# Performance work log

Measured on AMD Instinct MI355X. Metric: run time of the kernel, lower is better.

The kernel has to match this reference:

```python
import jax, jax.numpy as jnp
import numpy as np

EMBED_DIM = 128
NUM_HEADS = 4
WH, WW = 7, 7
N = WH * WW
HEAD_DIM = EMBED_DIM // NUM_HEADS
SCALE = HEAD_DIM ** -0.5


def _rel_position_index():
    # double_step_seq(2*Ww-1, Wh, 1, Ww), then idx = coords + coords.T, flip cols
    seq1 = np.arange(0, (2 * WW - 1) * WH, 2 * WW - 1)
    seq2 = np.arange(0, WW)
    coords = (seq1[:, None] + seq2[None, :]).reshape(1, -1)  # (1, N)
    idx = coords + coords.T                                   # (N, N)
    idx = idx[:, ::-1].copy()                                 # flip(1)
    return jnp.asarray(idx, dtype=jnp.int32)

REL_IDX = _rel_position_index()


def setup_inputs() -> dict:
    key = jax.random.key(0)
    ks = jax.random.split(key, 8)
    B = 4096
    nW = 64
    C = EMBED_DIM
    x = jax.random.normal(ks[0], (B, N, C), dtype=jnp.float32)
    # shift mask: values in (-inf, 0]; emulate with -100 on ~half the entries
    mask = jnp.where(jax.random.uniform(ks[1], (nW, N, N)) > 0.5, -100.0, 0.0).astype(jnp.float32)
    lim = 1.0 / np.sqrt(C)
    qkv_w = jax.random.uniform(ks[2], (3 * C, C), minval=-lim, maxval=lim, dtype=jnp.float32)
    qkv_b = jax.random.uniform(ks[3], (3 * C,), minval=-lim, maxval=lim, dtype=jnp.float32)
    proj_w = jax.random.uniform(ks[4], (C, C), minval=-lim, maxval=lim, dtype=jnp.float32)
    proj_b = jax.random.uniform(ks[5], (C,), minval=-lim, maxval=lim, dtype=jnp.float32)
    n_rel = (2 * WH - 1) * (2 * WW - 1)
    bias_table = 0.02 * jax.random.normal(ks[6], (n_rel, NUM_HEADS), dtype=jnp.float32)
    return {"x": x, "mask": mask, "qkv_w": qkv_w, "qkv_b": qkv_b,
            "proj_w": proj_w, "proj_b": proj_b, "bias_table": bias_table}


def reference(x, mask, qkv_w, qkv_b, proj_w, proj_b, bias_table):
    B, n, C = x.shape
    H, D = NUM_HEADS, HEAD_DIM
    qkv = x @ qkv_w.T + qkv_b                       # (B, N, 3C)
    qkv = qkv.reshape(B, n, 3, H, D).transpose(2, 0, 3, 1, 4)
    q, k, v = qkv[0], qkv[1], qkv[2]                # each (B, H, N, D)
    attn = jnp.einsum('bhnd,bhmd->bhnm', q * SCALE, k)
    # relative position bias gather: (N, N, H) -> (H, N, N)
    rel_bias = bias_table[REL_IDX.reshape(-1)].reshape(n, n, H).transpose(2, 0, 1)
    attn = attn + rel_bias[None]
    nW = mask.shape[0]
    attn = attn.reshape(B // nW, nW, H, n, n) + mask[None, :, None]
    attn = attn.reshape(B, H, n, n)
    attn = jax.nn.softmax(attn, axis=-1)
    out = jnp.einsum('bhnm,bhmd->bhnd', attn, v)    # (B, H, N, D)
    out = out.transpose(0, 2, 1, 3).reshape(B, n, C)
    return out @ proj_w.T + proj_b
```

## Files before the change

### kernel.cpp

```cpp
#include <hip/hip_runtime.h>


typedef __bf16 bf16_t;
typedef __bf16 bf8v  __attribute__((ext_vector_type(8)));
typedef __bf16 bf4v  __attribute__((ext_vector_type(4)));
typedef float  f4v   __attribute__((ext_vector_type(4)));

#define QK_SCALE 0.17677669529663687f

__device__ __forceinline__ f4v mfma16(bf8v a, bf8v b, f4v c) {
  return __builtin_amdgcn_mfma_f32_16x16x32_bf16(a, b, c, 0, 0, 0);
}

__device__ __forceinline__ bf8v join8(bf4v lo, bf4v hi) {
  return __builtin_shufflevector(lo, hi, 0, 1, 2, 3, 4, 5, 6, 7);
}

__global__ void prep_kernel(const float* __restrict__ mask,
                            const float* __restrict__ qkv_w,
                            const float* __restrict__ proj_w,
                            const float* __restrict__ bias_table,
                            bf16_t* __restrict__ wq,
                            bf16_t* __restrict__ wp,
                            float* __restrict__ cbs) {
  const int stride = gridDim.x * blockDim.x;
  const int tid0 = blockIdx.x * blockDim.x + threadIdx.x;
  for (int i = tid0; i < 24 * 4 * 64 * 8; i += stride) {
    int j = i & 7, l = (i >> 3) & 63, kt = (i >> 9) & 3, t = i >> 11;
    int n = t * 16 + (l & 15), k = kt * 32 + (l >> 4) * 8 + j;
    wq[i] = (bf16_t)qkv_w[n * 128 + k];
  }
  for (int i = tid0; i < 8 * 4 * 64 * 8; i += stride) {
    int j = i & 7, l = (i >> 3) & 63, kt = (i >> 9) & 3, t = i >> 11;
    int n = t * 16 + (l & 15), k = kt * 32 + (l >> 4) * 8 + j;
    wp[i] = (bf16_t)proj_w[n * 128 + k];
  }
  for (int i = tid0; i < 64 * 4 * 64 * 64; i += stride) {
    int j = i & 63;
    int l16 = j >> 2, nt = j & 3;
    int m = nt * 16 + l16;
    int n = (i >> 6) & 63, h = (i >> 12) & 3, w = i >> 14;
    float v;
    if (m >= 49) {
      v = -1e30f;
    } else if (n >= 49) {
      v = 0.0f;
    } else {
      int cn = 13 * (n / 7) + n % 7;
      int mm = 48 - m;
      int cm = 13 * (mm / 7) + mm % 7;
      v = bias_table[(cn + cm) * 4 + h] + mask[(w * 49 + n) * 49 + m];
    }
    cbs[i] = v;
  }
}

__global__ __launch_bounds__(256, 3) void msa_kernel(
    const float* __restrict__ x,
    const float* __restrict__ qkv_b,
    const float* __restrict__ proj_b,
    const bf16_t* __restrict__ wq,
    const bf16_t* __restrict__ wp,
    const float* __restrict__ cbs,
    float* __restrict__ out) {
  __shared__ __align__(16) bf16_t gA[8704];
  __shared__ __align__(16) bf16_t gB[4][4608];

#define AS(r, c)   gA[(r) * 136 + (c)]
#define VT(h, d, t) gA[((h) * 32 + (d)) * 68 + (t)]
#define QQ(h, r, d) gB[h][(r) * 36 + (d)]
#define KK(h, r, d) gB[h][2304 + (r) * 36 + (d)]
#define PP(h, n, m) gB[h][(n) * 72 + (m)]
#define OV(h, t, d) gB[h][(t) * 36 + (d)]

  const int tid = threadIdx.x;
  const int wv  = tid >> 6;
  const int ln  = tid & 63;
  const int l16 = ln & 15;
  const int l4  = ln >> 4;
  const int b   = blockIdx.x;
  const int w   = b & 63;

  {
    const float4* xb = (const float4*)(x + (size_t)b * (49 * 128));
    for (int i = tid; i < 64 * 32; i += 256) {
      int r = i >> 5, c4 = (i & 31) << 2;
      float4 v;
      if (r < 49) v = xb[(r * 128 + c4) >> 2];
      else        v = make_float4(0.f, 0.f, 0.f, 0.f);
      bf4v o = { (bf16_t)v.x, (bf16_t)v.y, (bf16_t)v.z, (bf16_t)v.w };
      *(bf4v*)&AS(r, c4) = o;
    }
  }
  __syncthreads();

  {
    f4v acc[4][6];
    for (int mt = 0; mt < 4; ++mt)
      for (int nj = 0; nj < 6; ++nj) acc[mt][nj] = (f4v){0.f, 0.f, 0.f, 0.f};
    for (int kt = 0; kt < 4; ++kt) {
      bf8v a[4];
      for (int mt = 0; mt < 4; ++mt)
        a[mt] = *(const bf8v*)&AS(mt * 16 + l16, kt * 32 + l4 * 8);
      bf8v bwv[6];
      for (int nj = 0; nj < 6; ++nj) {
        int t = wv * 6 + nj;
        bwv[nj] = *(const bf8v*)(wq + (((t * 4 + kt) * 64 + ln) << 3));
      }
      for (int mt = 0; mt < 4; ++mt)
        for (int nj = 0; nj < 6; ++nj)
          acc[mt][nj] = mfma16(a[mt], bwv[nj], acc[mt][nj]);
    }
    __syncthreads();
    for (int nj = 0; nj < 6; ++nj) {
      int t = wv * 6 + nj;
      int n0 = t * 16 + l16;
      float bias = qkv_b[n0];
      int sect = n0 >> 7;
      int h = (n0 & 127) >> 5;
      int d = n0 & 31;
      for (int mt = 0; mt < 4; ++mt) {
        int row0 = mt * 16 + l4 * 4;
        if (sect == 0) {
          for (int r = 0; r < 4; ++r)
            QQ(h, row0 + r, d) = (bf16_t)((acc[mt][nj][r] + bias) * QK_SCALE);
        } else if (sect == 1) {
          for (int r = 0; r < 4; ++r)
            KK(h, row0 + r, d) = (bf16_t)(acc[mt][nj][r] + bias);
        } else {
          bf4v o = { (bf16_t)(acc[mt][nj][0] + bias), (bf16_t)(acc[mt][nj][1] + bias),
                     (bf16_t)(acc[mt][nj][2] + bias), (bf16_t)(acc[mt][nj][3] + bias) };
          *(bf4v*)&VT(h, d, row0) = o;
        }
      }
    }
  }
  __syncthreads();

  {
    const int h = wv;
    f4v lg[4][4];
    bf8v qf[4], kf[4];
    for (int mt = 0; mt < 4; ++mt) {
      bf4v lo = *(const bf4v*)&QQ(h, mt * 16 + l16, l4 * 8);
      bf4v hi = *(const bf4v*)&QQ(h, mt * 16 + l16, l4 * 8 + 4);
      qf[mt] = join8(lo, hi);
    }
    for (int nt = 0; nt < 4; ++nt) {
      bf4v lo = *(const bf4v*)&KK(h, nt * 16 + l16, l4 * 8);
      bf4v hi = *(const bf4v*)&KK(h, nt * 16 + l16, l4 * 8 + 4);
      kf[nt] = join8(lo, hi);
    }
    for (int mt = 0; mt < 4; ++mt)
      for (int nt = 0; nt < 4; ++nt)
        lg[mt][nt] = mfma16(qf[mt], kf[nt], (f4v){0.f, 0.f, 0.f, 0.f});

    const float* cbp = cbs + ((size_t)(w * 4 + h) << 12);
    for (int mt = 0; mt < 4; ++mt) {
      for (int r = 0; r < 4; ++r) {
        int row = mt * 16 + l4 * 4 + r;
        float4 cbv = *(const float4*)(cbp + (row << 6) + l16 * 4);
        float vals[4];
        vals[0] = __expf(fmaxf(lg[mt][0][r] + cbv.x, -80.f));
        vals[1] = __expf(fmaxf(lg[mt][1][r] + cbv.y, -80.f));
        vals[2] = __expf(fmaxf(lg[mt][2][r] + cbv.z, -80.f));
        vals[3] = __expf(fmaxf(lg[mt][3][r] + cbv.w, -80.f));
        float s = (vals[0] + vals[1]) + (vals[2] + vals[3]);
        for (int off = 1; off < 16; off <<= 1) s += __shfl_xor(s, off);
        float inv = 1.0f / s;
        for (int nt = 0; nt < 4; ++nt)
          PP(h, row, nt * 16 + l16) = (bf16_t)(vals[nt] * inv);
      }
    }

    f4v oc[2][4];
    for (int mt = 0; mt < 2; ++mt)
      for (int nt = 0; nt < 4; ++nt) oc[mt][nt] = (f4v){0.f, 0.f, 0.f, 0.f};
    for (int ks = 0; ks < 2; ++ks) {
      bf8v vf[2], pf[4];
      for (int mt = 0; mt < 2; ++mt) {
        bf4v lo = *(const bf4v*)&VT(h, mt * 16 + l16, ks * 32 + l4 * 8);
        bf4v hi = *(const bf4v*)&VT(h, mt * 16 + l16, ks * 32 + l4 * 8 + 4);
        vf[mt] = join8(lo, hi);
      }
      for (int nt = 0; nt < 4; ++nt)
        pf[nt] = *(const bf8v*)&PP(h, nt * 16 + l16, ks * 32 + l4 * 8);
      for (int mt = 0; mt < 2; ++mt)
        for (int nt = 0; nt < 4; ++nt)
          oc[mt][nt] = mfma16(vf[mt], pf[nt], oc[mt][nt]);
    }
    for (int mt = 0; mt < 2; ++mt)
      for (int nt = 0; nt < 4; ++nt) {
        bf4v o = { (bf16_t)oc[mt][nt][0], (bf16_t)oc[mt][nt][1],
                   (bf16_t)oc[mt][nt][2], (bf16_t)oc[mt][nt][3] };
        *(bf4v*)&OV(h, nt * 16 + l16, mt * 16 + l4 * 4) = o;
      }
  }
  __syncthreads();

  {
    f4v acc[4][2];
    for (int mt = 0; mt < 4; ++mt)
      for (int nj = 0; nj < 2; ++nj) acc[mt][nj] = (f4v){0.f, 0.f, 0.f, 0.f};
    for (int kt = 0; kt < 4; ++kt) {
      bf8v a[4];
      for (int mt = 0; mt < 4; ++mt) {
        bf4v lo = *(const bf4v*)&OV(kt, mt * 16 + l16, l4 * 8);
        bf4v hi = *(const bf4v*)&OV(kt, mt * 16 + l16, l4 * 8 + 4);
        a[mt] = join8(lo, hi);
      }
      bf8v bwv[2];
      for (int nj = 0; nj < 2; ++nj) {
        int t = wv * 2 + nj;
        bwv[nj] = *(const bf8v*)(wp + (((t * 4 + kt) * 64 + ln) << 3));
      }
      for (int mt = 0; mt < 4; ++mt)
        for (int nj = 0; nj < 2; ++nj)
          acc[mt][nj] = mfma16(a[mt], bwv[nj], acc[mt][nj]);
    }
    float* ob = out + (size_t)b * (49 * 128);
    for (int nj = 0; nj < 2; ++nj) {
      int c = (wv * 2 + nj) * 16 + l16;
      float pb = proj_b[c];
      for (int mt = 0; mt < 4; ++mt) {
        for (int r = 0; r < 4; ++r) {
          int row = mt * 16 + l4 * 4 + r;
          if (row < 49) ob[row * 128 + c] = acc[mt][nj][r] + pb;
        }
      }
    }
  }
}

extern "C" void kernel_launch(void* const* d_in, const int* in_sizes, int n_in,
                              void* d_out, int out_size, void* d_ws, size_t ws_size,
                              hipStream_t stream) {
  const float* x          = (const float*)d_in[0];
  const float* mask       = (const float*)d_in[1];
  const float* qkv_w      = (const float*)d_in[2];
  const float* qkv_b      = (const float*)d_in[3];
  const float* proj_w     = (const float*)d_in[4];
  const float* proj_b     = (const float*)d_in[5];
  const float* bias_table = (const float*)d_in[6];

  char* ws = (char*)d_ws;
  bf16_t* wq = (bf16_t*)ws;
  bf16_t* wp = (bf16_t*)(ws + 98304);
  float*  cbs = (float*)(ws + 131072);

  prep_kernel<<<1024, 256, 0, stream>>>(mask, qkv_w, proj_w, bias_table, wq, wp, cbs);
  msa_kernel<<<4096, 256, 0, stream>>>(x, qkv_b, proj_b, wq, wp, cbs, (float*)d_out);
}
```

Before: 293.6 us.

## Assign QKV columns per head to each wave and swizzle shared-memory layouts

Each wave now computes the Q, K and V columns for its own head directly from x loaded from global memory into registers, instead of staging x in LDS and spreading QKV columns across waves. This removes the x staging buffer and two block-wide barriers, since each wave only reads its own head's LDS region until the projection stage. Padded LDS layouts are replaced with XOR-swizzled layouts so 16-byte fragment loads replace split 8-byte loads. Every wave now reads x from global or cache separately, and the qkv_b loads and LDS footprint change.

```diff
diff --git a/kernel.cpp b/kernel.cpp
--- a/kernel.cpp
+++ b/kernel.cpp
@@ -12,9 +12,9 @@
   return __builtin_amdgcn_mfma_f32_16x16x32_bf16(a, b, c, 0, 0, 0);
 }
 
-__device__ __forceinline__ bf8v join8(bf4v lo, bf4v hi) {
-  return __builtin_shufflevector(lo, hi, 0, 1, 2, 3, 4, 5, 6, 7);
-}
+#define QIX(row, d) ((row) * 32 + ((((((d) >> 3) ^ (((row) >> 1) & 3)) & 3)) << 3) + ((d) & 7))
+#define VIX(dd, t)  (4096 + (dd) * 64 + ((((((t) >> 3) ^ ((dd) & 7)) & 7)) << 3) + ((t) & 7))
+#define PIX(n, m)   ((n) * 64 + ((((((m) >> 3) ^ ((n) & 7)) & 7)) << 3) + ((m) & 7))
 
 __global__ void prep_kernel(const float* __restrict__ mask,
                             const float* __restrict__ qkv_w,
@@ -63,15 +63,7 @@
     const bf16_t* __restrict__ wp,
     const float* __restrict__ cbs,
     float* __restrict__ out) {
-  __shared__ __align__(16) bf16_t gA[8704];
-  __shared__ __align__(16) bf16_t gB[4][4608];
-
-#define AS(r, c)   gA[(r) * 136 + (c)]
-#define VT(h, d, t) gA[((h) * 32 + (d)) * 68 + (t)]
-#define QQ(h, r, d) gB[h][(r) * 36 + (d)]
-#define KK(h, r, d) gB[h][2304 + (r) * 36 + (d)]
-#define PP(h, n, m) gB[h][(n) * 72 + (m)]
-#define OV(h, t, d) gB[h][(t) * 36 + (d)]
+  __shared__ __align__(16) bf16_t gB[4][6144];
 
   const int tid = threadIdx.x;
   const int wv  = tid >> 6;
@@ -80,83 +72,90 @@
   const int l4  = ln >> 4;
   const int b   = blockIdx.x;
   const int w   = b & 63;
+  const int h   = wv;
+  bf16_t* S = gB[wv];
+
+  const int tg[6] = {2 * h, 2 * h + 1, 8 + 2 * h, 9 + 2 * h, 16 + 2 * h, 17 + 2 * h};
+  f4v acc[6][4];
+#pragma unroll
+  for (int g = 0; g < 6; ++g)
+#pragma unroll
+    for (int mt = 0; mt < 4; ++mt) acc[g][mt] = (f4v){0.f, 0.f, 0.f, 0.f};
+
+  const float* xb = x + (size_t)b * (49 * 128);
+#pragma unroll
+  for (int kt = 0; kt < 4; ++kt) {
+    bf8v a[4];
+#pragma unroll
+    for (int mt = 0; mt < 4; ++mt) {
+      int row = mt * 16 + l16;
+      f4v f0 = (f4v){0.f, 0.f, 0.f, 0.f}, f1 = (f4v){0.f, 0.f, 0.f, 0.f};
+      if (row < 49) {
+        const float* xr = xb + row * 128 + kt * 32 + l4 * 8;
+        f0 = *(const f4v*)xr;
+        f1 = *(const f4v*)(xr + 4);
+      }
+      bf8v av = { (bf16_t)f0[0], (bf16_t)f0[1], (bf16_t)f0[2], (bf16_t)f0[3],
+                  (bf16_t)f1[0], (bf16_t)f1[1], (bf16_t)f1[2], (bf16_t)f1[3] };
+      a[mt] = av;
+    }
+    bf8v bw[6];
+#pragma unroll
+    for (int g = 0; g < 6; ++g)
+      bw[g] = *(const bf8v*)(wq + (((tg[g] * 4 + kt) * 64 + ln) << 3));
+#pragma unroll
+    for (int g = 0; g < 6; ++g)
+#pragma unroll
+      for (int mt = 0; mt < 4; ++mt)
+        acc[g][mt] = mfma16(a[mt], bw[g], acc[g][mt]);
+  }
+
+#pragma unroll
+  for (int g = 0; g < 4; ++g) {
+    float bias = qkv_b[tg[g] * 16 + l16];
+    int d = ((g & 1) << 4) + l16;
+    int base = (g < 2) ? 0 : 2048;
+    float scale = (g < 2) ? QK_SCALE : 1.0f;
+#pragma unroll
+    for (int mt = 0; mt < 4; ++mt)
+#pragma unroll
+      for (int r = 0; r < 4; ++r) {
+        int row = mt * 16 + l4 * 4 + r;
+        S[base + QIX(row, d)] = (bf16_t)((acc[g][mt][r] + bias) * scale);
+      }
+  }
+#pragma unroll
+  for (int g = 4; g < 6; ++g) {
+    float bias = qkv_b[tg[g] * 16 + l16];
+    int d = ((g & 1) << 4) + l16;
+#pragma unroll
+    for (int mt = 0; mt < 4; ++mt) {
+      int t0 = mt * 16 + l4 * 4;
+      bf4v o = { (bf16_t)(acc[g][mt][0] + bias), (bf16_t)(acc[g][mt][1] + bias),
+                 (bf16_t)(acc[g][mt][2] + bias), (bf16_t)(acc[g][mt][3] + bias) };
+      *(bf4v*)&S[VIX(d, t0)] = o;
+    }
+  }
 
   {
-    const float4* xb = (const float4*)(x + (size_t)b * (49 * 128));
-    for (int i = tid; i < 64 * 32; i += 256) {
-      int r = i >> 5, c4 = (i & 31) << 2;
-      float4 v;
-      if (r < 49) v = xb[(r * 128 + c4) >> 2];
-      else        v = make_float4(0.f, 0.f, 0.f, 0.f);
-      bf4v o = { (bf16_t)v.x, (bf16_t)v.y, (bf16_t)v.z, (bf16_t)v.w };
-      *(bf4v*)&AS(r, c4) = o;
-    }
-  }
-  __syncthreads();
-
-  {
-    f4v acc[4][6];
-    for (int mt = 0; mt < 4; ++mt)
-      for (int nj = 0; nj < 6; ++nj) acc[mt][nj] = (f4v){0.f, 0.f, 0.f, 0.f};
-    for (int kt = 0; kt < 4; ++kt) {
-      bf8v a[4];
-      for (int mt = 0; mt < 4; ++mt)
-        a[mt] = *(const bf8v*)&AS(mt * 16 + l16, kt * 32 + l4 * 8);
-      bf8v bwv[6];
-      for (int nj = 0; nj < 6; ++nj) {
-        int t = wv * 6 + nj;
-        bwv[nj] = *(const bf8v*)(wq + (((t * 4 + kt) * 64 + ln) << 3));
-      }
-      for (int mt = 0; mt < 4; ++mt)
-        for (int nj = 0; nj < 6; ++nj)
-          acc[mt][nj] = mfma16(a[mt], bwv[nj], acc[mt][nj]);
-    }
-    __syncthreads();
-    for (int nj = 0; nj < 6; ++nj) {
-      int t = wv * 6 + nj;
-      int n0 = t * 16 + l16;
-      float bias = qkv_b[n0];
-      int sect = n0 >> 7;
-      int h = (n0 & 127) >> 5;
-      int d = n0 & 31;
-      for (int mt = 0; mt < 4; ++mt) {
-        int row0 = mt * 16 + l4 * 4;
-        if (sect == 0) {
-          for (int r = 0; r < 4; ++r)
-            QQ(h, row0 + r, d) = (bf16_t)((acc[mt][nj][r] + bias) * QK_SCALE);
-        } else if (sect == 1) {
-          for (int r = 0; r < 4; ++r)
-            KK(h, row0 + r, d) = (bf16_t)(acc[mt][nj][r] + bias);
-        } else {
-          bf4v o = { (bf16_t)(acc[mt][nj][0] + bias), (bf16_t)(acc[mt][nj][1] + bias),
-                     (bf16_t)(acc[mt][nj][2] + bias), (bf16_t)(acc[mt][nj][3] + bias) };
-          *(bf4v*)&VT(h, d, row0) = o;
-        }
-      }
-    }
-  }
-  __syncthreads();
-
-  {
-    const int h = wv;
     f4v lg[4][4];
     bf8v qf[4], kf[4];
-    for (int mt = 0; mt < 4; ++mt) {
-      bf4v lo = *(const bf4v*)&QQ(h, mt * 16 + l16, l4 * 8);
-      bf4v hi = *(const bf4v*)&QQ(h, mt * 16 + l16, l4 * 8 + 4);
-      qf[mt] = join8(lo, hi);
-    }
-    for (int nt = 0; nt < 4; ++nt) {
-      bf4v lo = *(const bf4v*)&KK(h, nt * 16 + l16, l4 * 8);
-      bf4v hi = *(const bf4v*)&KK(h, nt * 16 + l16, l4 * 8 + 4);
-      kf[nt] = join8(lo, hi);
-    }
+#pragma unroll
+    for (int mt = 0; mt < 4; ++mt) {
+      int row = mt * 16 + l16;
+      qf[mt] = *(const bf8v*)&S[QIX(row, l4 * 8)];
+      kf[mt] = *(const bf8v*)&S[2048 + QIX(row, l4 * 8)];
+    }
+#pragma unroll
     for (int mt = 0; mt < 4; ++mt)
+#pragma unroll
       for (int nt = 0; nt < 4; ++nt)
         lg[mt][nt] = mfma16(qf[mt], kf[nt], (f4v){0.f, 0.f, 0.f, 0.f});
 
     const float* cbp = cbs + ((size_t)(w * 4 + h) << 12);
-    for (int mt = 0; mt < 4; ++mt) {
+#pragma unroll
+    for (int mt = 0; mt < 4; ++mt) {
+#pragma unroll
       for (int r = 0; r < 4; ++r) {
         int row = mt * 16 + l4 * 4 + r;
         float4 cbv = *(const float4*)(cbp + (row << 6) + l16 * 4);
@@ -166,68 +165,83 @@
         vals[2] = __expf(fmaxf(lg[mt][2][r] + cbv.z, -80.f));
         vals[3] = __expf(fmaxf(lg[mt][3][r] + cbv.w, -80.f));
         float s = (vals[0] + vals[1]) + (vals[2] + vals[3]);
+#pragma unroll
         for (int off = 1; off < 16; off <<= 1) s += __shfl_xor(s, off);
         float inv = 1.0f / s;
+#pragma unroll
         for (int nt = 0; nt < 4; ++nt)
-          PP(h, row, nt * 16 + l16) = (bf16_t)(vals[nt] * inv);
+          S[PIX(row, nt * 16 + l16)] = (bf16_t)(vals[nt] * inv);
       }
     }
 
     f4v oc[2][4];
+#pragma unroll
     for (int mt = 0; mt < 2; ++mt)
+#pragma unroll
       for (int nt = 0; nt < 4; ++nt) oc[mt][nt] = (f4v){0.f, 0.f, 0.f, 0.f};
+#pragma unroll
     for (int ks = 0; ks < 2; ++ks) {
       bf8v vf[2], pf[4];
-      for (int mt = 0; mt < 2; ++mt) {
-        bf4v lo = *(const bf4v*)&VT(h, mt * 16 + l16, ks * 32 + l4 * 8);
-        bf4v hi = *(const bf4v*)&VT(h, mt * 16 + l16, ks * 32 + l4 * 8 + 4);
-        vf[mt] = join8(lo, hi);
-      }
+#pragma unroll
+      for (int mt = 0; mt < 2; ++mt)
+        vf[mt] = *(const bf8v*)&S[VIX(mt * 16 + l16, ks * 32 + l4 * 8)];
+#pragma unroll
       for (int nt = 0; nt < 4; ++nt)
-        pf[nt] = *(const bf8v*)&PP(h, nt * 16 + l16, ks * 32 + l4 * 8);
+        pf[nt] = *(const bf8v*)&S[PIX(nt * 16 + l16, ks * 32 + l4 * 8)];
+#pragma unroll
       for (int mt = 0; mt < 2; ++mt)
+#pragma unroll
         for (int nt = 0; nt < 4; ++nt)
           oc[mt][nt] = mfma16(vf[mt], pf[nt], oc[mt][nt]);
     }
+#pragma unroll
     for (int mt = 0; mt < 2; ++mt)
+#pragma unroll
       for (int nt = 0; nt < 4; ++nt) {
+        int n = nt * 16 + l16, d0 = mt * 16 + l4 * 4;
         bf4v o = { (bf16_t)oc[mt][nt][0], (bf16_t)oc[mt][nt][1],
                    (bf16_t)oc[mt][nt][2], (bf16_t)oc[mt][nt][3] };
-        *(bf4v*)&OV(h, nt * 16 + l16, mt * 16 + l4 * 4) = o;
+        *(bf4v*)&S[QIX(n, d0)] = o;
       }
   }
   __syncthreads();
 
   {
-    f4v acc[4][2];
-    for (int mt = 0; mt < 4; ++mt)
-      for (int nj = 0; nj < 2; ++nj) acc[mt][nj] = (f4v){0.f, 0.f, 0.f, 0.f};
+    f4v pacc[2][4];
+#pragma unroll
+    for (int nj = 0; nj < 2; ++nj)
+#pragma unroll
+      for (int mt = 0; mt < 4; ++mt) pacc[nj][mt] = (f4v){0.f, 0.f, 0.f, 0.f};
+#pragma unroll
     for (int kt = 0; kt < 4; ++kt) {
       bf8v a[4];
-      for (int mt = 0; mt < 4; ++mt) {
-        bf4v lo = *(const bf4v*)&OV(kt, mt * 16 + l16, l4 * 8);
-        bf4v hi = *(const bf4v*)&OV(kt, mt * 16 + l16, l4 * 8 + 4);
-        a[mt] = join8(lo, hi);
-      }
-      bf8v bwv[2];
+#pragma unroll
+      for (int mt = 0; mt < 4; ++mt)
+        a[mt] = *(const bf8v*)&gB[kt][QIX(mt * 16 + l16, l4 * 8)];
+      bf8v bw[2];
+#pragma unroll
       for (int nj = 0; nj < 2; ++nj) {
         int t = wv * 2 + nj;
-        bwv[nj] = *(const bf8v*)(wp + (((t * 4 + kt) * 64 + ln) << 3));
-      }
-      for (int mt = 0; mt < 4; ++mt)
-        for (int nj = 0; nj < 2; ++nj)
-          acc[mt][nj] = mfma16(a[mt], bwv[nj], acc[mt][nj]);
+        bw[nj] = *(const bf8v*)(wp + (((t * 4 + kt) * 64 + ln) << 3));
+      }
+#pragma unroll
+      for (int nj = 0; nj < 2; ++nj)
+#pragma unroll
+        for (int mt = 0; mt < 4; ++mt)
+          pacc[nj][mt] = mfma16(a[mt], bw[nj], pacc[nj][mt]);
     }
     float* ob = out + (size_t)b * (49 * 128);
+#pragma unroll
     for (int nj = 0; nj < 2; ++nj) {
       int c = (wv * 2 + nj) * 16 + l16;
       float pb = proj_b[c];
-      for (int mt = 0; mt < 4; ++mt) {
+#pragma unroll
+      for (int mt = 0; mt < 4; ++mt)
+#pragma unroll
         for (int r = 0; r < 4; ++r) {
           int row = mt * 16 + l4 * 4 + r;
-          if (row < 49) ob[row * 128 + c] = acc[mt][nj][r] + pb;
+          if (row < 49) ob[row * 128 + c] = pacc[nj][mt][r] + pb;
         }
-      }
     }
   }
 }
```

Result: slower. 326.4 us (+11.2%).
